# Kernel optimization log

Measured on AMD Instinct MI355X. Metric: run time of the kernel, lower is better.

## Reference

```python
import jax, jax.numpy as jnp
import numpy as np

N, C, T, V = 32, 64, 512, 25
CO = 64            # out_channels
C4 = CO // 4       # inter channel (conv_a/conv_d output, kc//3)
W3 = 3 * V         # unfolded node dim
BN_EPS = 1e-5


def setup_inputs() -> dict:
    key = jax.random.key(0)
    ks = jax.random.split(key, 12)
    s = 0.05
    return {
        "x": jax.random.normal(ks[0], (N, C, T, V), dtype=jnp.float32),
        "A": jax.random.uniform(ks[1], (3, W3, W3), dtype=jnp.float32) * 0.1,  # fixed adjacency buffer
        "PA": jnp.full((3, W3, W3), 1e-6, dtype=jnp.float32),                   # learned adjacency offset
        "conv_a_w": jax.random.normal(ks[2], (C4, C), dtype=jnp.float32) * s,   # 1x1 conv_a[0]
        "conv_a_b": jnp.zeros((C4,), dtype=jnp.float32),
        "conv_d_w": jax.random.normal(ks[3], (C4, C), dtype=jnp.float32) * s,   # 1x1 conv_d[0]
        "conv_d_b": jnp.zeros((C4,), dtype=jnp.float32),
        "conv_w": jax.random.normal(ks[4], (3 * C4, C), dtype=jnp.float32) * s, # main 1x1 conv (t_kernel_size=1)
        "conv_b": jnp.zeros((3 * C4,), dtype=jnp.float32),
        "out_w": jax.random.normal(ks[5], (CO, C4, 3), dtype=jnp.float32) * s,  # conv3d kernel (1,3,1)
        "out_b": jnp.zeros((CO,), dtype=jnp.float32),
        "bn_gamma": jnp.ones((CO,), dtype=jnp.float32),
        "bn_beta": jnp.zeros((CO,), dtype=jnp.float32),
        "bn_mean": jnp.zeros((CO,), dtype=jnp.float32),
        "bn_var": jnp.ones((CO,), dtype=jnp.float32),
    }


def _unfold3(x):
    # UnfoldTemporalWindows(3,1,1): (N,C,T,V) -> (N,C,T,3V), zero-pad T by 1
    n, c, t, v = x.shape
    xp = jnp.pad(x, ((0, 0), (0, 0), (1, 1), (0, 0)))
    win = jnp.stack([xp[:, :, i:i + t, :] for i in range(3)], axis=3)  # (N,C,T,3,V)
    return win.reshape(n, c, t, 3 * v)


def reference(x, A, PA, conv_a_w, conv_a_b, conv_d_w, conv_d_b,
              conv_w, conv_b, out_w, out_b, bn_gamma, bn_beta, bn_mean, bn_var):
    n, c, t, v = x.shape
    w3 = 3 * v
    Aeff = A + PA  # (3, 3V, 3V)

    x2 = _unfold3(x)  # (N,C,T,3V)

    # adaptive graph attention: matmul-softmax-matmul
    a1 = jnp.einsum('nctw,oc->notw', x2, conv_a_w) + conv_a_b[None, :, None, None]  # (N,C4,T,3V)
    a11 = a1.transpose(0, 3, 1, 2).reshape(n, w3, -1)   # (N,3V,C4*T)
    a2 = a1.reshape(n, -1, w3)                          # (N,C4*T,3V)
    att = jax.nn.softmax(jnp.matmul(a11, a2) / w3, axis=-2)  # (N,3V,3V), softmax over dim -2
    xz = jnp.matmul(x2.reshape(n, c * t, w3), att).reshape(n, c, t, w3)
    z = jnp.einsum('nctw,oc->notw', xz, conv_d_w) + conv_d_b[None, :, None, None]  # (N,C4,T,3V)

    # main branch: 1x1 conv -> split into k=3 -> einsum graph conv with A
    x1 = jnp.einsum('nctw,oc->notw', x2, conv_w) + conv_b[None, :, None, None]  # (N,3*C4,T,3V)
    c4 = conv_d_w.shape[0]
    x1 = x1.reshape(n, 3, c4, t, w3)
    x1 = jnp.einsum('nkctv,kvw->nctw', x1, Aeff)  # (N,C4,T,3V)
    x1 = x1 + z

    # conv3d (1,3,1) collapses the window-of-3 dim
    x1 = x1.reshape(n, c4, t, 3, v)
    y = jnp.einsum('nctwv,ocw->notv', x1, out_w) + out_b[None, :, None, None]  # (N,CO,T,V)

    # BatchNorm2d (inference form)
    inv = jax.lax.rsqrt(bn_var + BN_EPS)
    y = (y - bn_mean[None, :, None, None]) * (bn_gamma * inv)[None, :, None, None] + bn_beta[None, :, None, None]

    y = y + x  # in_channels == out_channels -> identity residual
    return jax.nn.relu(y)
```

## Files before the change

### kernel.cpp

```cpp
#include <hip/hip_runtime.h>
#include <hip/hip_bf16.h>


typedef unsigned short u16;
typedef unsigned int   u32;
typedef __attribute__((ext_vector_type(8))) short bf16x8;
typedef __attribute__((ext_vector_type(4))) float f32x4;

__device__ __forceinline__ float b2f(u32 u) {
    union { u32 i; float f; } x; x.i = (u & 0xffffu) << 16; return x.f;
}
__device__ __forceinline__ u16 f2b(float f) {
    union { float f; u32 i; } x; x.f = f;
    u32 i = x.i;
    return (u16)((i + 0x7fffu + ((i >> 16) & 1u)) >> 16);
}
__device__ __forceinline__ u32 pack2(float a, float b) {
    return (u32)f2b(a) | ((u32)f2b(b) << 16);
}
__device__ __forceinline__ void unpack8(uint4 u, float* f) {
    f[0] = b2f(u.x); f[1] = b2f(u.x >> 16);
    f[2] = b2f(u.y); f[3] = b2f(u.y >> 16);
    f[4] = b2f(u.z); f[5] = b2f(u.z >> 16);
    f[6] = b2f(u.w); f[7] = b2f(u.w >> 16);
}

__global__ __launch_bounds__(256) void k0_bta(
    const float* __restrict__ A, const float* __restrict__ PA,
    u16* __restrict__ BtA)
{
    int e = blockIdx.x * 256 + threadIdx.x;
    if (e >= 80 * 288) return;
    int w = e / 288, k = e - w * 288;
    int r = k >> 5, v = k & 31, g = r / 3, i = r - g * 3;
    float val = 0.f;
    if (v < 25 && w < 75) {
        int idx = (g * 75 + i * 25 + v) * 75 + w;
        val = A[idx] + PA[idx];
    }
    BtA[e] = f2b(val);
}

__global__ __launch_bounds__(256, 2) void k1_conv80(
    const float* __restrict__ x,
    const float* __restrict__ wa, const float* __restrict__ ba,
    const float* __restrict__ wd, const float* __restrict__ bd,
    const float* __restrict__ wc, const float* __restrict__ bc,
    u16* __restrict__ a1o, u16* __restrict__ hcn)
{
    __shared__ __align__(16) u16 Xt[256 * 64];
    __shared__ __align__(16) u16 Csh[80 * 264];
    char* XtB = (char*)Xt;

    const int b    = blockIdx.x;
    const int n    = b >> 4;
    const int t0   = (b & 15) << 5;
    const int tid  = threadIdx.x;
    const int wave = tid >> 6, lane = tid & 63;
    const int q    = lane >> 4, r = lane & 15;

    bf16x8 wfrag[5][2];
    float  breg[5];
    #pragma unroll
    for (int mt = 0; mt < 5; ++mt) {
        const int o = mt * 16 + r;
        const float* src = (o < 16) ? (wa + o * 64)
                         : (o < 32) ? (wd + (o - 16) * 64)
                                    : (wc + (o - 32) * 64);
        breg[mt] = (o < 16) ? ba[o] : (o < 32) ? bd[o - 16] : bc[o - 32];
        #pragma unroll
        for (int ks = 0; ks < 2; ++ks) {
            bf16x8 f;
            #pragma unroll
            for (int j = 0; j < 8; ++j)
                f[j] = (short)f2b(src[ks * 32 + q * 8 + j]);
            wfrag[mt][ks] = f;
        }
    }

    if (t0 == 0) {
        uint4 z; z.x = 0u; z.y = 0u; z.z = 0u; z.w = 0u;
        for (int e = tid; e < 50; e += 256)
            *(uint4*)&a1o[((size_t)n * 514) * 400 + e * 8] = z;
    }
    if (t0 == 480) {
        uint4 z; z.x = 0u; z.y = 0u; z.z = 0u; z.w = 0u;
        for (int e = tid; e < 50; e += 256)
            *(uint4*)&a1o[((size_t)n * 514 + 513) * 400 + e * 8] = z;
    }

    {
        uint4 z; z.x = 0u; z.y = 0u; z.z = 0u; z.w = 0u;
        for (int e = tid; e < 448; e += 256) {
            const int pc = e >> 3, ch = e & 7;
            const int tl = pc / 7, pv = pc - tl * 7;
            const int col = tl * 32 + 25 + pv;
            *(uint4*)(XtB + col * 128 + ch * 16) = z;
        }
    }

    auto epilogue = [&](int tbp) {
        for (int e = tid; e < 2048; e += 256) {
            const int cc  = e >> 5;
            const int rem = e & 31;
            const int tl  = rem >> 2, v0 = (rem & 3) << 3;
            const int o   = (cc < 48) ? cc + 32 : cc - 32;
            uint4 pk = *(const uint4*)&Csh[o * 264 + tl * 32 + v0];
            *(uint4*)&hcn[(((size_t)n * 64 + cc) * 512 + (tbp + tl)) * 32 + v0] = pk;
        }
        for (int e = tid; e < 400; e += 256) {
            const int tv = e >> 1, h = (e & 1) << 3;
            const int tl = (tv * 41) >> 10;
            const int v  = tv - tl * 25;
            const int cb = tl * 32 + v;
            u16 a[8];
            #pragma unroll
            for (int k = 0; k < 8; ++k) a[k] = Csh[(h + k) * 264 + cb];
            uint4 pk;
            pk.x = (u32)a[0] | ((u32)a[1] << 16);
            pk.y = (u32)a[2] | ((u32)a[3] << 16);
            pk.z = (u32)a[4] | ((u32)a[5] << 16);
            pk.w = (u32)a[6] | ((u32)a[7] << 16);
            *(uint4*)&a1o[(((size_t)n * 514 + (tbp + tl + 1)) * 25 + v) * 16 + h] = pk;
        }
    };

    for (int s = 0; s < 4; ++s) {
        const int tb = t0 + s * 8;

        if (s > 0) epilogue(tb - 8);
        for (int e = tid; e < 400; e += 256) {
            const int co = e / 50;
            const int tq = e - co * 50;
            const float* gp = x + (((size_t)n * 64 + co * 8) * 512 + tb) * 25 + tq * 4;
            float fl[32];
            #pragma unroll
            for (int i = 0; i < 8; ++i) {
                const float4 t4 = *(const float4*)(gp + (size_t)i * 12800);
                fl[i * 4 + 0] = t4.x; fl[i * 4 + 1] = t4.y;
                fl[i * 4 + 2] = t4.z; fl[i * 4 + 3] = t4.w;
            }
            #pragma unroll
            for (int j = 0; j < 4; ++j) {
                const int tv  = tq * 4 + j;
                const int tl  = (tv * 41) >> 10;
                const int col = tl * 32 + (tv - tl * 25);
                uint4 pk;
                pk.x = pack2(fl[0 * 4 + j], fl[1 * 4 + j]);
                pk.y = pack2(fl[2 * 4 + j], fl[3 * 4 + j]);
                pk.z = pack2(fl[4 * 4 + j], fl[5 * 4 + j]);
                pk.w = pack2(fl[6 * 4 + j], fl[7 * 4 + j]);
                *(uint4*)(XtB + col * 128 + ((co * 16) ^ ((col & 7) << 4))) = pk;
            }
        }
        __syncthreads();

        {
            f32x4 acc[4][5];
            #pragma unroll
            for (int a_ = 0; a_ < 4; ++a_)
                #pragma unroll
                for (int m_ = 0; m_ < 5; ++m_)
                    acc[a_][m_] = (f32x4){0.f, 0.f, 0.f, 0.f};

            #pragma unroll
            for (int nt4 = 0; nt4 < 4; ++nt4) {
                const int col = (wave * 4 + nt4) * 16 + r;
                const int swz = (col & 7) << 4;
                const char* rowp = (const char*)Xt + col * 128;
                const bf16x8 x0 = *(const bf16x8*)(rowp + ((q * 16) ^ swz));
                const bf16x8 x1 = *(const bf16x8*)(rowp + ((64 + q * 16) ^ swz));
                #pragma unroll
                for (int mt = 0; mt < 5; ++mt) {
                    acc[nt4][mt] = __builtin_amdgcn_mfma_f32_16x16x32_bf16(
                        x0, wfrag[mt][0], acc[nt4][mt], 0, 0, 0);
                    acc[nt4][mt] = __builtin_amdgcn_mfma_f32_16x16x32_bf16(
                        x1, wfrag[mt][1], acc[nt4][mt], 0, 0, 0);
                }
            }
            #pragma unroll
            for (int nt4 = 0; nt4 < 4; ++nt4) {
                const int colb = (wave * 4 + nt4) * 16 + q * 4;
                #pragma unroll
                for (int mt = 0; mt < 5; ++mt) {
                    const int o = mt * 16 + r;
                    const float bi = breg[mt];
                    uint2 pr;
                    pr.x = pack2(acc[nt4][mt][0] + bi, acc[nt4][mt][1] + bi);
                    pr.y = pack2(acc[nt4][mt][2] + bi, acc[nt4][mt][3] + bi);
                    *(uint2*)&Csh[o * 264 + colb] = pr;
                }
            }
        }
        __syncthreads();
    }
    epilogue(t0 + 24);
}

__global__ __launch_bounds__(256, 2) void k2a_mfma(
    const u16* __restrict__ a1o, float* __restrict__ Spart)
{
    __shared__ u16 U[80 * 136];
    __shared__ float Sred[80 * 80];
    const int b   = blockIdx.x;
    const int n   = b >> 4;
    const int tc  = b & 15;
    const int t0  = tc * 32;
    const int tid = threadIdx.x;
    const int wave = tid >> 6, lane = tid & 63;
    const int q = lane >> 4, col = lane & 15;

    f32x4 acc[25];
    #pragma unroll
    for (int i = 0; i < 25; ++i) acc[i] = (f32x4){0.f, 0.f, 0.f, 0.f};

    for (int s = 0; s < 4; ++s) {
        __syncthreads();
        for (int e = tid; e < 1280; e += 256) {
            int row = e >> 4, c8 = (e & 15) << 3;
            uint4 val; val.x = 0u; val.y = 0u; val.z = 0u; val.w = 0u;
            if (row < 75) {
                int i = row / 25, v = row - i * 25;
                int tl = c8 >> 4, o0 = c8 & 8;
                int tp = t0 + s * 8 + tl + i;
                val = *(const uint4*)&a1o[(((size_t)n * 514 + tp) * 25 + v) * 16 + o0];
            }
            *(uint4*)&U[row * 136 + c8] = val;
        }
        __syncthreads();

        const int k0 = wave * 32 + q * 8;
        bf16x8 fr[5];
        #pragma unroll
        for (int r = 0; r < 5; ++r)
            fr[r] = *(const bf16x8*)&U[(r * 16 + col) * 136 + k0];
        #pragma unroll
        for (int mt = 0; mt < 5; ++mt)
            #pragma unroll
            for (int nt = 0; nt < 5; ++nt)
                acc[mt * 5 + nt] = __builtin_amdgcn_mfma_f32_16x16x32_bf16(
                    fr[mt], fr[nt], acc[mt * 5 + nt], 0, 0, 0);
    }

    for (int w = 0; w < 4; ++w) {
        if (wave == w) {
            #pragma unroll
            for (int mt = 0; mt < 5; ++mt)
                #pragma unroll
                for (int nt = 0; nt < 5; ++nt)
                    #pragma unroll
                    for (int reg = 0; reg < 4; ++reg) {
                        int idx = (mt * 16 + q * 4 + reg) * 80 + nt * 16 + col;
                        if (w == 0) Sred[idx]  = acc[mt * 5 + nt][reg];
                        else        Sred[idx] += acc[mt * 5 + nt][reg];
                    }
        }
        __syncthreads();
    }
    float* dst = &Spart[(size_t)(n * 16 + tc) * 6400];
    for (int e = tid; e < 6400; e += 256) dst[e] = Sred[e];
}

__global__ __launch_bounds__(256) void k2b_softmax(
    const float* __restrict__ Spart, u16* __restrict__ BtT)
{
    __shared__ float S[6400];
    const int n = blockIdx.x, tid = threadIdx.x;
    for (int e = tid; e < 6400; e += 256) {
        float s = 0.f;
        for (int ks = 0; ks < 16; ++ks)
            s += Spart[(size_t)(n * 16 + ks) * 6400 + e];
        S[e] = s * (1.0f / 75.0f);
    }
    __syncthreads();
    if (tid < 80) {
        const int w2 = tid;
        float r = 0.f;
        if (w2 < 75) {
            float m = -1e30f;
            for (int w1 = 0; w1 < 75; ++w1) m = fmaxf(m, S[w1 * 80 + w2]);
            float s = 0.f;
            for (int w1 = 0; w1 < 75; ++w1) {
                float e = __expf(S[w1 * 80 + w2] - m);
                S[w1 * 80 + w2] = e;
                s += e;
            }
            r = 1.0f / s;
        }
        for (int k = 0; k < 96; ++k) {
            int i = k >> 5, v = k & 31;
            float val = (w2 < 75 && v < 25) ? S[(i * 25 + v) * 80 + w2] * r : 0.f;
            BtT[((size_t)n * 80 + w2) * 96 + k] = f2b(val);
        }
    }
}

__global__ __launch_bounds__(256, 2) void k3_graph(
    const u16* __restrict__ hcn, const u16* __restrict__ BtA,
    const u16* __restrict__ BtT, u16* __restrict__ sum12)
{
    __shared__ u16 Bt[80 * 392];
    const int b    = blockIdx.x;
    const int n    = b >> 4;
    const int tblk = (b & 15) << 5;
    const int tid  = threadIdx.x;

    for (int e = tid; e < 3840; e += 256) {
        int row = e / 48, cs = e - row * 48;
        uint4 val;
        if (cs < 36) val = *(const uint4*)&BtA[row * 288 + cs * 8];
        else         val = *(const uint4*)&BtT[((size_t)n * 80 + row) * 96 + (cs - 36) * 8];
        *(uint4*)&Bt[row * 392 + cs * 8] = val;
    }
    __syncthreads();

    const int wave = tid >> 6, lane = tid & 63;
    const int c = lane & 15, q = lane >> 4;
    const int tb = tblk + wave * 8;

    for (int tt = 0; tt < 8; tt += 2) {
        const int t0 = tb + tt, t1 = t0 + 1;
        bf16x8 a0[12], a1[12];
        #pragma unroll
        for (int r = 0; r < 12; ++r) {
            const int g = r / 3, i = r - g * 3;
            const size_t rowb = ((size_t)n * 64 + g * 16 + c) * 512;
            const int tp0 = t0 + i - 1, tp1 = t1 + i - 1;
            a0[r] = (tp0 >= 0 && tp0 < 512)
                  ? *(const bf16x8*)&hcn[(rowb + tp0) * 32 + q * 8] : (bf16x8)(short)0;
            a1[r] = (tp1 >= 0 && tp1 < 512)
                  ? *(const bf16x8*)&hcn[(rowb + tp1) * 32 + q * 8] : (bf16x8)(short)0;
        }
        #pragma unroll 1
        for (int nt = 0; nt < 5; ++nt) {
            f32x4 acc0 = {0.f, 0.f, 0.f, 0.f};
            f32x4 acc1 = {0.f, 0.f, 0.f, 0.f};
            const u16* bp = &Bt[(nt * 16 + c) * 392 + q * 8];
            #pragma unroll
            for (int r = 0; r < 12; ++r) {
                bf16x8 bf = *(const bf16x8*)(bp + r * 32);
                acc0 = __builtin_amdgcn_mfma_f32_16x16x32_bf16(a0[r], bf, acc0, 0, 0, 0);
                acc1 = __builtin_amdgcn_mfma_f32_16x16x32_bf16(a1[r], bf, acc1, 0, 0, 0);
            }
            const size_t ob0 = (((size_t)n * 512 + t0) * 16) * 80 + nt * 16 + c;
            const size_t ob1 = (((size_t)n * 512 + t1) * 16) * 80 + nt * 16 + c;
            #pragma unroll
            for (int reg = 0; reg < 4; ++reg) {
                sum12[ob0 + (size_t)(q * 4 + reg) * 80] = f2b(acc0[reg]);
                sum12[ob1 + (size_t)(q * 4 + reg) * 80] = f2b(acc1[reg]);
            }
        }
    }
}

__global__ __launch_bounds__(256) void k4_out(
    const u16* __restrict__ sum12,
    const float* __restrict__ ow, const float* __restrict__ obias,
    const float* __restrict__ bg, const float* __restrict__ bb,
    const float* __restrict__ bm, const float* __restrict__ bv,
    const float* __restrict__ x, float* __restrict__ out)
{
    __shared__ float ss[4][16][3][28];
    const int b   = blockIdx.x;
    const int n   = b >> 7;
    const int t0  = (b & 127) << 2;
    const int tid = threadIdx.x;
    const int o   = tid & 63;
    const int ts  = tid >> 6;

    float* sf = &ss[0][0][0][0];
    for (int e = tid; e < 4 * 16 * 3 * 28; e += 256) sf[e] = 0.f;
    __syncthreads();
    for (int e = tid; e < 4 * 16 * 75; e += 256) {
        int ts2 = e / 1200, r = e - ts2 * 1200;
        int c = r / 75, w = r - c * 75;
        int ww = w / 25, v = w - ww * 25;
        ss[ts2][c][ww][v] =
            b2f(sum12[(((size_t)n * 512 + t0 + ts2) * 16 + c) * 80 + w]);
    }
    __syncthreads();

    float wreg[48];
    #pragma unroll
    for (int k = 0; k < 48; ++k) wreg[k] = ow[o * 48 + k];
    const float scale = bg[o] * rsqrtf(bv[o] + 1e-5f);
    const float shift = bb[o] - bm[o] * scale;
    const float obv   = obias[o];

    float accs[25];
    #pragma unroll
    for (int v = 0; v < 25; ++v) accs[v] = 0.f;

    for (int c = 0; c < 16; ++c) {
        #pragma unroll
        for (int ww = 0; ww < 3; ++ww) {
            const float wv = wreg[c * 3 + ww];
            const float* sp = &ss[ts][c][ww][0];
            #pragma unroll
            for (int j = 0; j < 6; ++j) {
                float4 s4 = *(const float4*)&sp[j * 4];
                accs[j * 4 + 0] = fmaf(wv, s4.x, accs[j * 4 + 0]);
                accs[j * 4 + 1] = fmaf(wv, s4.y, accs[j * 4 + 1]);
                accs[j * 4 + 2] = fmaf(wv, s4.z, accs[j * 4 + 2]);
                accs[j * 4 + 3] = fmaf(wv, s4.w, accs[j * 4 + 3]);
            }
            accs[24] = fmaf(wv, sp[24], accs[24]);
        }
    }

    const int t = t0 + ts;
    const size_t base = (((size_t)n * 64 + o) * 512 + t) * 25;
    #pragma unroll
    for (int v = 0; v < 25; ++v) {
        float y = (accs[v] + obv) * scale + shift + x[base + v];
        out[base + v] = fmaxf(y, 0.f);
    }
}

extern "C" void kernel_launch(void* const* d_in, const int* in_sizes, int n_in,
                              void* d_out, int out_size, void* d_ws, size_t ws_size,
                              hipStream_t stream)
{
    const float* x  = (const float*)d_in[0];
    const float* A  = (const float*)d_in[1];
    const float* PA = (const float*)d_in[2];
    const float* wa = (const float*)d_in[3];
    const float* ba = (const float*)d_in[4];
    const float* wd = (const float*)d_in[5];
    const float* bd = (const float*)d_in[6];
    const float* wc = (const float*)d_in[7];
    const float* bc = (const float*)d_in[8];
    const float* ow = (const float*)d_in[9];
    const float* ob = (const float*)d_in[10];
    const float* bg = (const float*)d_in[11];
    const float* bb = (const float*)d_in[12];
    const float* bm = (const float*)d_in[13];
    const float* bv = (const float*)d_in[14];
    float* out = (float*)d_out;

    char* ws = (char*)d_ws;
    u16*   a1o   = (u16*)(ws);
    u16*   hcn   = (u16*)(ws + 13158400);
    u16*   sum12 = (u16*)(ws + 80267264);
    u16*   BtA   = (u16*)(ws + 122210304);
    u16*   BtT   = (u16*)(ws + 122256384);
    float* Spart = (float*)(ws + 122747904);

    k0_bta    <<<90,   256, 0, stream>>>(A, PA, BtA);
    k1_conv80 <<<512,  256, 0, stream>>>(x, wa, ba, wd, bd, wc, bc, a1o, hcn);
    k2a_mfma  <<<512,  256, 0, stream>>>(a1o, Spart);
    k2b_softmax<<<32,  256, 0, stream>>>(Spart, BtT);
    k3_graph  <<<512,  256, 0, stream>>>(hcn, BtA, BtT, sum12);
    k4_out    <<<4096, 256, 0, stream>>>(sum12, ow, ob, bg, bb, bm, bv, x, out);
}
```

Baseline: 454.4 us.

## Rewrite output conv3d+BN epilogue with MFMA and a (t,v)-major sum12 layout

k3_graph now writes sum12 in a per-(t,v) layout with the 16 channels × 3 window entries contiguous (48 wide, padded to 1536 per t), dropping padded columns. k4_out loads 8 timesteps per block into a swizzled LDS tile and computes the 64×48 output projection with bf16 MFMA instead of scalar FMAs, then applies bias, BN, residual and ReLU. Spart now shares workspace with sum12. Quantizing the conv3d weights to bf16 adds some rounding error, and the output stores from the MFMA layout may be less coalesced.

```diff
diff --git a/kernel.cpp b/kernel.cpp
--- a/kernel.cpp
+++ b/kernel.cpp
@@ -342,78 +342,133 @@
                 acc0 = __builtin_amdgcn_mfma_f32_16x16x32_bf16(a0[r], bf, acc0, 0, 0, 0);
                 acc1 = __builtin_amdgcn_mfma_f32_16x16x32_bf16(a1[r], bf, acc1, 0, 0, 0);
             }
-            const size_t ob0 = (((size_t)n * 512 + t0) * 16) * 80 + nt * 16 + c;
-            const size_t ob1 = (((size_t)n * 512 + t1) * 16) * 80 + nt * 16 + c;
-            #pragma unroll
-            for (int reg = 0; reg < 4; ++reg) {
-                sum12[ob0 + (size_t)(q * 4 + reg) * 80] = f2b(acc0[reg]);
-                sum12[ob1 + (size_t)(q * 4 + reg) * 80] = f2b(acc1[reg]);
-            }
-        }
-    }
-}
-
-__global__ __launch_bounds__(256) void k4_out(
+            const int w = nt * 16 + c;
+            if (w < 75) {
+                const int ww = (w >= 50) ? 2 : ((w >= 25) ? 1 : 0);
+                const int v  = w - ww * 25;
+                const size_t b0 = ((size_t)n * 512 + t0) * 1536 + v * 48 + q * 12 + ww;
+                const size_t b1 = ((size_t)n * 512 + t1) * 1536 + v * 48 + q * 12 + ww;
+                #pragma unroll
+                for (int reg = 0; reg < 4; ++reg) {
+                    sum12[b0 + (size_t)(reg * 3)] = f2b(acc0[reg]);
+                    sum12[b1 + (size_t)(reg * 3)] = f2b(acc1[reg]);
+                }
+            }
+        }
+    }
+}
+
+__global__ __launch_bounds__(256, 2) void k4_out(
     const u16* __restrict__ sum12,
     const float* __restrict__ ow, const float* __restrict__ obias,
     const float* __restrict__ bg, const float* __restrict__ bb,
     const float* __restrict__ bm, const float* __restrict__ bv,
     const float* __restrict__ x, float* __restrict__ out)
 {
-    __shared__ float ss[4][16][3][28];
-    const int b   = blockIdx.x;
-    const int n   = b >> 7;
-    const int t0  = (b & 127) << 2;
-    const int tid = threadIdx.x;
-    const int o   = tid & 63;
-    const int ts  = tid >> 6;
-
-    float* sf = &ss[0][0][0][0];
-    for (int e = tid; e < 4 * 16 * 3 * 28; e += 256) sf[e] = 0.f;
+    __shared__ __align__(16) u16 Bsh[256 * 64];
+    char* BshB = (char*)Bsh;
+    const int b    = blockIdx.x;
+    const int n    = b >> 6;
+    const int t0   = (b & 63) << 3;
+    const int tid  = threadIdx.x;
+    const int wave = tid >> 6, lane = tid & 63;
+    const int q    = lane >> 4, c15 = lane & 15;
+
+    {
+        uint4 z; z.x = 0u; z.y = 0u; z.z = 0u; z.w = 0u;
+        for (int e = tid; e < 960; e += 256) {
+            int col, j;
+            if (e < 512) { col = e >> 1; j = 6 + (e & 1); }
+            else {
+                const int r2 = e - 512;
+                const int cc = r2 >> 3; j = r2 & 7;
+                const int tl = cc / 7, pv = cc - tl * 7;
+                col = tl * 32 + 25 + pv;
+            }
+            *(uint4*)(BshB + col * 128 + ((j * 16) ^ ((col & 7) << 4))) = z;
+        }
+    }
+    for (int e = tid; e < 1200; e += 256) {
+        const int j  = e % 6;
+        const int rv = e / 6;
+        const int tl = (rv * 41) >> 10;
+        const int v  = rv - tl * 25;
+        const uint4 val = *(const uint4*)
+            &sum12[((size_t)n * 512 + t0 + tl) * 1536 + v * 48 + j * 8];
+        const int col = tl * 32 + v;
+        *(uint4*)(BshB + col * 128 + ((j * 16) ^ ((col & 7) << 4))) = val;
+    }
+
+    bf16x8 wfrag[4][2];
+    #pragma unroll
+    for (int mt = 0; mt < 4; ++mt) {
+        const int o = mt * 16 + c15;
+        #pragma unroll
+        for (int ks = 0; ks < 2; ++ks) {
+            bf16x8 f;
+            #pragma unroll
+            for (int j = 0; j < 8; ++j) {
+                const int k = ks * 32 + q * 8 + j;
+                f[j] = (k < 48) ? (short)f2b(ow[o * 48 + k]) : (short)0;
+            }
+            wfrag[mt][ks] = f;
+        }
+    }
+    float scl[4][4], shf[4][4], obv[4][4];
+    #pragma unroll
+    for (int mt = 0; mt < 4; ++mt)
+        #pragma unroll
+        for (int reg = 0; reg < 4; ++reg) {
+            const int o = mt * 16 + q * 4 + reg;
+            const float s = bg[o] * rsqrtf(bv[o] + 1e-5f);
+            scl[mt][reg] = s;
+            shf[mt][reg] = bb[o] - bm[o] * s;
+            obv[mt][reg] = obias[o];
+        }
     __syncthreads();
-    for (int e = tid; e < 4 * 16 * 75; e += 256) {
-        int ts2 = e / 1200, r = e - ts2 * 1200;
-        int c = r / 75, w = r - c * 75;
-        int ww = w / 25, v = w - ww * 25;
-        ss[ts2][c][ww][v] =
-            b2f(sum12[(((size_t)n * 512 + t0 + ts2) * 16 + c) * 80 + w]);
-    }
-    __syncthreads();
-
-    float wreg[48];
-    #pragma unroll
-    for (int k = 0; k < 48; ++k) wreg[k] = ow[o * 48 + k];
-    const float scale = bg[o] * rsqrtf(bv[o] + 1e-5f);
-    const float shift = bb[o] - bm[o] * scale;
-    const float obv   = obias[o];
-
-    float accs[25];
-    #pragma unroll
-    for (int v = 0; v < 25; ++v) accs[v] = 0.f;
-
-    for (int c = 0; c < 16; ++c) {
-        #pragma unroll
-        for (int ww = 0; ww < 3; ++ww) {
-            const float wv = wreg[c * 3 + ww];
-            const float* sp = &ss[ts][c][ww][0];
-            #pragma unroll
-            for (int j = 0; j < 6; ++j) {
-                float4 s4 = *(const float4*)&sp[j * 4];
-                accs[j * 4 + 0] = fmaf(wv, s4.x, accs[j * 4 + 0]);
-                accs[j * 4 + 1] = fmaf(wv, s4.y, accs[j * 4 + 1]);
-                accs[j * 4 + 2] = fmaf(wv, s4.z, accs[j * 4 + 2]);
-                accs[j * 4 + 3] = fmaf(wv, s4.w, accs[j * 4 + 3]);
-            }
-            accs[24] = fmaf(wv, sp[24], accs[24]);
-        }
-    }
-
-    const int t = t0 + ts;
-    const size_t base = (((size_t)n * 64 + o) * 512 + t) * 25;
-    #pragma unroll
-    for (int v = 0; v < 25; ++v) {
-        float y = (accs[v] + obv) * scale + shift + x[base + v];
-        out[base + v] = fmaxf(y, 0.f);
+
+    f32x4 acc[4][4];
+    #pragma unroll
+    for (int ct = 0; ct < 4; ++ct)
+        #pragma unroll
+        for (int mt = 0; mt < 4; ++mt)
+            acc[ct][mt] = (f32x4){0.f, 0.f, 0.f, 0.f};
+
+    const int wb = wave * 64;
+    #pragma unroll
+    for (int ct = 0; ct < 4; ++ct) {
+        const int col = wb + ct * 16 + c15;
+        const int swz = (col & 7) << 4;
+        const char* rp = BshB + col * 128;
+        const bf16x8 b0 = *(const bf16x8*)(rp + ((q * 16) ^ swz));
+        const bf16x8 b1 = *(const bf16x8*)(rp + ((64 + q * 16) ^ swz));
+        #pragma unroll
+        for (int mt = 0; mt < 4; ++mt) {
+            acc[ct][mt] = __builtin_amdgcn_mfma_f32_16x16x32_bf16(
+                wfrag[mt][0], b0, acc[ct][mt], 0, 0, 0);
+            acc[ct][mt] = __builtin_amdgcn_mfma_f32_16x16x32_bf16(
+                wfrag[mt][1], b1, acc[ct][mt], 0, 0, 0);
+        }
+    }
+
+    #pragma unroll
+    for (int ct = 0; ct < 4; ++ct) {
+        const int col = wb + ct * 16 + c15;
+        const int tl = col >> 5, v = col & 31;
+        if (v < 25) {
+            const int t = t0 + tl;
+            #pragma unroll
+            for (int mt = 0; mt < 4; ++mt) {
+                #pragma unroll
+                for (int reg = 0; reg < 4; ++reg) {
+                    const int o = mt * 16 + q * 4 + reg;
+                    const size_t idx = (((size_t)n * 64 + o) * 512 + t) * 25 + v;
+                    const float y = (acc[ct][mt][reg] + obv[mt][reg]) * scl[mt][reg]
+                                    + shf[mt][reg] + x[idx];
+                    out[idx] = fmaxf(y, 0.f);
+                }
+            }
+        }
     }
 }
 
@@ -442,14 +497,14 @@
     u16*   a1o   = (u16*)(ws);
     u16*   hcn   = (u16*)(ws + 13158400);
     u16*   sum12 = (u16*)(ws + 80267264);
-    u16*   BtA   = (u16*)(ws + 122210304);
-    u16*   BtT   = (u16*)(ws + 122256384);
-    float* Spart = (float*)(ws + 122747904);
+    float* Spart = (float*)(ws + 80267264);
+    u16*   BtA   = (u16*)(ws + 130598912);
+    u16*   BtT   = (u16*)(ws + 130644992);
 
     k0_bta    <<<90,   256, 0, stream>>>(A, PA, BtA);
     k1_conv80 <<<512,  256, 0, stream>>>(x, wa, ba, wd, bd, wc, bc, a1o, hcn);
     k2a_mfma  <<<512,  256, 0, stream>>>(a1o, Spart);
     k2b_softmax<<<32,  256, 0, stream>>>(Spart, BtT);
     k3_graph  <<<512,  256, 0, stream>>>(hcn, BtA, BtT, sum12);
-    k4_out    <<<4096, 256, 0, stream>>>(sum12, ow, ob, bg, bb, bm, bv, x, out);
-}
+    k4_out    <<<4096 / 2, 256, 0, stream>>>(sum12, ow, ob, bg, bb, bm, bv, x, out);
+}
```

New measurement: 470.7 us. 3.6% more time.
